# Optimization experiments

Measured on AMD Instinct MI355X. Metric: run time of the kernel, lower is better.

## Reference

```python
import jax, jax.numpy as jnp
import numpy as np

B, K, N, DIM, C_IN = 4, 2048, 4096, 3, 61
IN = DIM + C_IN        # 64, deepset input size
H1, H2 = 128, 128      # neighbor_xf hidden sizes
OUT = 64               # c_out // heads
HEADS = 4
EPS = 1e-5             # BatchNorm eps


def _lin(key, i, o):
    return jax.random.normal(key, (i, o), jnp.float32) * (1.0 / np.sqrt(i))


def setup_inputs() -> dict:
    key = jax.random.key(0)
    ks = jax.random.split(key, 12)
    return {
        "keys": jax.random.normal(ks[0], (B, K, DIM), jnp.float32),
        "points": jax.random.normal(ks[1], (B, N, DIM), jnp.float32),
        "feats": jax.random.normal(ks[2], (B, N, C_IN), jnp.float32),
        "nx_w1": _lin(ks[3], IN, H1), "nx_b1": jnp.zeros((H1,), jnp.float32),
        "nx_w2": _lin(ks[4], H1, H2), "nx_b2": jnp.zeros((H2,), jnp.float32),
        "nx_w3": _lin(ks[5], H2, OUT), "nx_b3": jnp.zeros((OUT,), jnp.float32),
        "sx_w1": _lin(ks[6], IN, IN), "sx_b1": jnp.zeros((IN,), jnp.float32),
        "sx_w2": _lin(ks[7], IN, IN), "sx_b2": jnp.zeros((IN,), jnp.float32),
        "sx_w3": _lin(ks[8], IN, IN), "sx_b3": jnp.zeros((IN,), jnp.float32),
        "att_w": _lin(ks[9], 2 * IN, HEADS * IN),
        "att_b": jnp.zeros((HEADS * IN,), jnp.float32),
        "att_q": jax.random.normal(ks[10], (HEADS, IN), jnp.float32) * 0.1,
        "bn_gamma": jnp.ones((IN,), jnp.float32),
        "bn_beta": jnp.zeros((IN,), jnp.float32),
        "neighbors": 32,
    }


def _mlp3(x, w1, b1, w2, b2, w3, b3):
    # per-element deepset MLP: Linear-ReLU-Linear-ReLU-Linear
    h = jax.nn.relu(x @ w1 + b1)
    h = jax.nn.relu(h @ w2 + b2)
    return h @ w3 + b3


def _forward(keys, points, feats, nx_w1, nx_b1, nx_w2, nx_b2, nx_w3, nx_b3,
             sx_w1, sx_b1, sx_w2, sx_b2, sx_w3, sx_b3,
             att_w, att_b, att_q, bn_gamma, bn_beta, neighbors):
    b = keys.shape[0]
    # Euclidean dist_fn: dist_vec [B,K,N,dim], dist [B,K,N], all points valid
    rel = points[:, None, :, :] - keys[:, :, None, :]
    dist = jnp.sqrt(jnp.sum(rel * rel, axis=-1))
    _, idx = jax.lax.top_k(-dist, neighbors)                   # [B,K,k] nearest
    nrel = jnp.take_along_axis(rel, idx[..., None], axis=2)    # [B,K,k,dim]
    bidx = jnp.arange(b)[:, None, None]
    nfeat = feats[bidx, idx]                                   # [B,K,k,c_in]
    comb = jnp.concatenate([nrel, nfeat], axis=-1)             # [B,K,k,in]
    lat = _mlp3(comb, nx_w1, nx_b1, nx_w2, nx_b2, nx_w3, nx_b3)  # [B,K,k,out]
    # BatchNorm1d (training-mode batch stats) over flattened [B*K*k, in]
    flat = comb.reshape(-1, comb.shape[-1])
    mean = jnp.mean(flat, axis=0)
    var = jnp.var(flat, axis=0)
    norm = (comb - mean) * jax.lax.rsqrt(var + EPS) * bn_gamma + bn_beta
    # SelfAttention: deepset sum-pooled context + per-neighbor softmax weights
    set_feat = jnp.sum(_mlp3(norm, sx_w1, sx_b1, sx_w2, sx_b2, sx_w3, sx_b3), axis=2)
    comb_feat = jnp.concatenate(
        [norm, jnp.broadcast_to(set_feat[:, :, None, :], norm.shape)], axis=-1)
    heads = (comb_feat @ att_w + att_b).reshape(comb_feat.shape[:3] + (HEADS, -1))
    e = jnp.sum(heads * att_q, axis=-1)                        # [B,K,k,H]
    w = jax.nn.softmax(e, axis=-2)                             # softmax over neighbor axis
    out = jnp.einsum('bkno,bknh->bkoh', lat, w)                # weighted reduce over k
    return out.reshape(out.shape[:2] + (-1,))                  # [B,K,out*H]


def reference(keys, points, feats, nx_w1, nx_b1, nx_w2, nx_b2, nx_w3, nx_b3,
              sx_w1, sx_b1, sx_w2, sx_b2, sx_w3, sx_b3,
              att_w, att_b, att_q, bn_gamma, bn_beta, neighbors):
    return _forward(keys, points, feats, nx_w1, nx_b1, nx_w2, nx_b2, nx_w3, nx_b3,
                    sx_w1, sx_b1, sx_w2, sx_b2, sx_w3, sx_b3,
                    att_w, att_b, att_q, bn_gamma, bn_beta, neighbors)
```

## Files before the change

kernel.cpp:

```cpp
#include <hip/hip_runtime.h>
#include <math.h>

#define BATCH 4
#define KQ    2048
#define NPTS  4096
#define CIN   61
#define KNN   32
#define ROWS  (BATCH*KQ*KNN)

#define OFF_IDX  0
#define OFF_ACC  524288
#define OFF_ATTA 557056
#define OFF_W1F  558080
#define OFF_W2F  574464
#define OFF_W3F  607232

typedef __attribute__((ext_vector_type(8)))  short bfrag;
typedef __attribute__((ext_vector_type(16))) float cfrag;

__device__ __forceinline__ unsigned short bf16_rne(float x) {
  unsigned u = __float_as_uint(x);
  unsigned r = u + 0x7fffu + ((u >> 16) & 1u);
  return (unsigned short)(r >> 16);
}
__device__ __forceinline__ float4 ld4u(const float* p) {
  float4 r; __builtin_memcpy(&r, p, 16); return r;
}

#define NCAND 320

template<int NS>
__device__ __forceinline__ void select_emit(
    const unsigned* __restrict__ VAL, const int* __restrict__ IDXL,
    int mcount, unsigned hib, int lane, int wid,
    const float* __restrict__ Pb, float kx, float ky, float kz,
    unsigned short* __restrict__ dst, int* __restrict__ SEL,
    float* __restrict__ accs) {
  const unsigned long long lmask = (1ull << lane) - 1ull;
  unsigned e[NS];
#pragma unroll
  for (int s = 0; s < NS; ++s) {
    int ei = s*64 + lane;
    e[s] = (ei < mcount) ? VAL[ei] : 0xffffffffu;
  }
  unsigned lo2 = e[0];
#pragma unroll
  for (int s = 1; s < NS; ++s) lo2 = min(lo2, e[s]);
#pragma unroll
  for (int off = 1; off < 64; off <<= 1)
    lo2 = min(lo2, (unsigned)__shfl_xor((int)lo2, off));
  unsigned hi2 = hib;
  while (lo2 < hi2) {
    unsigned mid = lo2 + ((hi2 - lo2) >> 1);
    int c = 0;
#pragma unroll
    for (int s = 0; s < NS; ++s) c += (int)__popcll(__ballot(e[s] <= mid));
    if (c == KNN) { hi2 = mid; break; }
    if (c > KNN) hi2 = mid; else lo2 = mid + 1;
  }
  const unsigned T = hi2;
  float r0=0.f,r1=0.f,r2=0.f,r3=0.f,r4=0.f,r5=0.f;
  int base2 = 0;
#pragma unroll
  for (int s = 0; s < NS; ++s) {
    bool p = (e[s] <= T);
    unsigned long long m = __ballot(p);
    if (p) {
      int pos = base2 + (int)__popcll(m & lmask);
      if (pos < KNN) {
        int n = IDXL[s*64 + lane];
        SEL[pos] = n;
        if (wid == 0) {
          dst[pos] = (unsigned short)n;
          float dx = Pb[n*3+0]-kx, dy = Pb[n*3+1]-ky, dz = Pb[n*3+2]-kz;
          r0 += dx; r1 += dy; r2 += dz;
          r3 += dx*dx; r4 += dy*dy; r5 += dz*dz;
        }
      }
    }
    base2 += (int)__popcll(m);
  }
  if (wid == 0) {
#pragma unroll
    for (int off = 32; off > 0; off >>= 1) {
      r0 += __shfl_down(r0, off); r1 += __shfl_down(r1, off);
      r2 += __shfl_down(r2, off); r3 += __shfl_down(r3, off);
      r4 += __shfl_down(r4, off); r5 += __shfl_down(r5, off);
    }
    if (lane == 0) {
      atomicAdd(&accs[0], r0); atomicAdd(&accs[1], r1); atomicAdd(&accs[2], r2);
      atomicAdd(&accs[64], r3); atomicAdd(&accs[65], r4); atomicAdd(&accs[66], r5);
    }
  }
}

__global__ __launch_bounds__(256, 8) void topk_kernel(
    const float* __restrict__ keys, const float* __restrict__ points,
    const float* __restrict__ feats,
    const float* __restrict__ w1, const float* __restrict__ w2,
    const float* __restrict__ w3,
    const float* __restrict__ att_w, const float* __restrict__ att_q,
    unsigned short* __restrict__ idx_out, float* __restrict__ acc,
    short* __restrict__ w1f, short* __restrict__ w2f, short* __restrict__ w3f,
    float* __restrict__ attA) {
  if (blockIdx.x >= 8192) {
    const int bb = blockIdx.x - 8192;
    if (bb == 128) {
      const int t = threadIdx.x, c = t >> 2, h = t & 3;
      float s = 0.f;
      for (int d = 0; d < 64; ++d) s += att_w[c*256 + h*64 + d] * att_q[h*64 + d];
      attA[c*4 + h] = s;
      return;
    }
    int t = bb * 256 + threadIdx.x;
    if (t < 8192) {
      int j = t & 7, lane = (t >> 3) & 63, tk = t >> 9;
      int kc = tk & 3, tile = tk >> 2;
      int nh = tile*32 + (lane & 31), k = kc*16 + (lane >> 5)*8 + j;
      w1f[t] = (short)bf16_rne(w1[k*128 + nh]);
    } else if (t < 24576) {
      int t2 = t - 8192;
      int j = t2 & 7, lane = (t2 >> 3) & 63, tk = t2 >> 9;
      int kc = tk & 7, tile = tk >> 3;
      int nh = tile*32 + (lane & 31), k = kc*16 + (lane >> 5)*8 + j;
      w2f[t2] = (short)bf16_rne(w2[k*128 + nh]);
    } else {
      int t3 = t - 24576;
      int j = t3 & 7, lane = (t3 >> 3) & 63, tk = t3 >> 9;
      int kc = tk & 7, tile = tk >> 3;
      int nh = tile*32 + (lane & 31), k = kc*16 + (lane >> 5)*8 + j;
      w3f[t3] = (short)bf16_rne(w3[k*64 + nh]);
    }
    return;
  }

  __shared__ unsigned VAL[NCAND];
  __shared__ int IDXL[NCAND];
  __shared__ int SEL[32];
  __shared__ unsigned HIW[4];
  __shared__ int WTOT[4];
  __shared__ float FRED[64*33];
  __shared__ float FQ[64*33];
  const int tid = threadIdx.x;
  const int lane = tid & 63, wid = tid >> 6;
  const int g = blockIdx.x;
  const int b = g >> 11;
  const float kx = keys[(size_t)g*3+0];
  const float ky = keys[(size_t)g*3+1];
  const float kz = keys[(size_t)g*3+2];
  const float* __restrict__ Pb = points + (size_t)b * NPTS * 3;

  unsigned u[16];
  unsigned lmin = 0xffffffffu;
#pragma unroll
  for (int c4 = 0; c4 < 4; ++c4) {
    const float* pp = Pb + (size_t)(tid*16 + c4*4) * 3;
    float4 A = ld4u(pp), B = ld4u(pp + 4), C = ld4u(pp + 8);
    float dx, dy, dz;
    dx = A.x-kx; dy = A.y-ky; dz = A.z-kz;
    u[c4*4+0] = __float_as_uint(dx*dx + dy*dy + dz*dz);
    dx = A.w-kx; dy = B.x-ky; dz = B.y-kz;
    u[c4*4+1] = __float_as_uint(dx*dx + dy*dy + dz*dz);
    dx = B.z-kx; dy = B.w-ky; dz = C.x-kz;
    u[c4*4+2] = __float_as_uint(dx*dx + dy*dy + dz*dz);
    dx = C.y-kx; dy = C.z-ky; dz = C.w-kz;
    u[c4*4+3] = __float_as_uint(dx*dx + dy*dy + dz*dz);
#pragma unroll
    for (int j = 0; j < 4; ++j) lmin = min(lmin, u[c4*4+j]);
  }
  unsigned wlo = lmin, whi = lmin;
#pragma unroll
  for (int off = 1; off < 64; off <<= 1) {
    unsigned a = (unsigned)__shfl_xor((int)wlo, off);
    unsigned bmx = (unsigned)__shfl_xor((int)whi, off);
    wlo = min(wlo, a); whi = max(whi, bmx);
  }
  unsigned lo = wlo, hi = whi;
  while (lo < hi) {
    unsigned mid = lo + ((hi - lo) >> 1);
    int c = (int)__popcll(__ballot(lmin <= mid));
    if (c == KNN) { hi = mid; break; }
    if (c > KNN) hi = mid; else lo = mid + 1;
  }
  if (lane == 0) HIW[wid] = hi;
  __syncthreads();
  const unsigned hib = min(min(HIW[0],HIW[1]), min(HIW[2],HIW[3]));

  int cnt = 0;
#pragma unroll
  for (int j = 0; j < 16; ++j) cnt += (u[j] <= hib) ? 1 : 0;
  int inc = cnt;
#pragma unroll
  for (int off = 1; off < 64; off <<= 1) {
    int t = __shfl_up(inc, off);
    if (lane >= off) inc += t;
  }
  if (lane == 63) WTOT[wid] = inc;
  __syncthreads();
  int base = inc - cnt;
  for (int w = 0; w < wid; ++w) base += WTOT[w];
  {
    int p = base;
#pragma unroll
    for (int j = 0; j < 16; ++j) {
      if (u[j] <= hib) {
        if (p < NCAND) { VAL[p] = u[j]; IDXL[p] = tid*16 + j; }
        ++p;
      }
    }
  }
  __syncthreads();
  const int mcount = min(WTOT[0]+WTOT[1]+WTOT[2]+WTOT[3], NCAND);

  {
    unsigned short* dst = idx_out + (size_t)g * KNN;
    float* accs = &acc[(g & 63)*128];
    if (mcount <= 64)
      select_emit<1>(VAL, IDXL, mcount, hib, lane, wid, Pb, kx, ky, kz, dst, SEL, accs);
    else if (mcount <= 128)
      select_emit<2>(VAL, IDXL, mcount, hib, lane, wid, Pb, kx, ky, kz, dst, SEL, accs);
    else
      select_emit<5>(VAL, IDXL, mcount, hib, lane, wid, Pb, kx, ky, kz, dst, SEL, accs);
  }

  {
    const int row = tid >> 3, chunk = tid & 7;
    const int n = SEL[row];
    const float* frow = feats + ((size_t)b*NPTS + n)*CIN;
    float fs[8] = {0,0,0,0,0,0,0,0}, fq[8] = {0,0,0,0,0,0,0,0};
    if (chunk < 7) {
      float4 a = ld4u(frow + chunk*8);
      float4 c4 = ld4u(frow + chunk*8 + 4);
      fs[0]=a.x;  fq[0]=a.x*a.x;   fs[1]=a.y;  fq[1]=a.y*a.y;
      fs[2]=a.z;  fq[2]=a.z*a.z;   fs[3]=a.w;  fq[3]=a.w*a.w;
      fs[4]=c4.x; fq[4]=c4.x*c4.x; fs[5]=c4.y; fq[5]=c4.y*c4.y;
      fs[6]=c4.z; fq[6]=c4.z*c4.z; fs[7]=c4.w; fq[7]=c4.w*c4.w;
    } else {
      float v0=frow[56], v1=frow[57], v2=frow[58], v3=frow[59], v4=frow[60];
      fs[0]=v0; fq[0]=v0*v0; fs[1]=v1; fq[1]=v1*v1;
      fs[2]=v2; fq[2]=v2*v2; fs[3]=v3; fq[3]=v3*v3;
      fs[4]=v4; fq[4]=v4*v4;
    }
#pragma unroll
    for (int i = 0; i < 8; ++i) {
      FRED[(chunk*8 + i)*33 + row] = fs[i];
      FQ  [(chunk*8 + i)*33 + row] = fq[i];
    }
  }
  __syncthreads();
  if (tid < 64) {
    float s = 0.f, q2 = 0.f;
#pragma unroll
    for (int r = 0; r < 32; ++r) {
      s  += FRED[tid*33 + r];
      q2 += FQ[tid*33 + r];
    }
    if (tid < CIN) {
      float* a = &acc[(g & 63)*128];
      atomicAdd(&a[3 + tid], s);
      atomicAdd(&a[64 + 3 + tid], q2);
    }
  }
}

#define L_W1F 0
#define L_W2F 16384
#define L_W3F 49152
#define L_B1  65536
#define L_B2  66048
#define L_B3  66560
#define L_AE  66816
#define L_ACT 67840
#define L_EPX 137472
#define L_TOT 145664

template<int KC, bool F32OUT>
__device__ __forceinline__ void gemm_part(const short* WF,
    const float* BIAS, short* ACTq, float* LATq,
    const bfrag* B, int tile0, int ntiles, int m, int q, int lane) {
#pragma unroll
  for (int t = 0; t < ntiles; ++t) {
    const int tile = tile0 + t;
    cfrag acc;
#pragma unroll
    for (int i = 0; i < 16; ++i) acc[i] = 0.f;
#pragma unroll
    for (int kc = 0; kc < KC; ++kc) {
      bfrag a = *(const bfrag*)(WF + ((tile*KC + kc)*64 + lane)*8);
      acc = __builtin_amdgcn_mfma_f32_32x32x16_bf16(a, B[kc], acc, 0, 0, 0);
    }
#pragma unroll
    for (int p = 0; p < 4; ++p) {
      const int nh = tile*32 + p*8 + q*4;
      float4 bv = *(const float4*)(BIAS + nh);
      if (F32OUT) {
        float4 o;
        o.x = acc[4*p+0] + bv.x; o.y = acc[4*p+1] + bv.y;
        o.z = acc[4*p+2] + bv.z; o.w = acc[4*p+3] + bv.w;
        *(float4*)(LATq + m*68 + nh) = o;
      } else {
        short4 s;
        s.x = (short)bf16_rne(fmaxf(acc[4*p+0] + bv.x, 0.f));
        s.y = (short)bf16_rne(fmaxf(acc[4*p+1] + bv.y, 0.f));
        s.z = (short)bf16_rne(fmaxf(acc[4*p+2] + bv.z, 0.f));
        s.w = (short)bf16_rne(fmaxf(acc[4*p+3] + bv.w, 0.f));
        *(short4*)(ACTq + m*136 + nh) = s;
      }
    }
  }
}

__global__ __launch_bounds__(1024, 4) void main_kernel(
    const float* __restrict__ keys, const float* __restrict__ points,
    const float* __restrict__ feats, const unsigned short* __restrict__ idxg,
    const short* __restrict__ w1f, const short* __restrict__ w2f,
    const short* __restrict__ w3f,
    const float* __restrict__ b1, const float* __restrict__ b2,
    const float* __restrict__ b3,
    const float* __restrict__ attAg, const float* __restrict__ accg,
    const float* __restrict__ gammav, float* __restrict__ out) {
  __shared__ __align__(16) char smem[L_TOT];
  const int tid = threadIdx.x;
  const int bid = blockIdx.x;
  const int wid = tid >> 6, lane = tid & 63;
  const int pairq = wid >> 1, wv = wid & 1;
  const int m = lane & 31, q = lane >> 5;

  short* SW1 = (short*)(smem + L_W1F);
  short* SW2 = (short*)(smem + L_W2F);
  short* SW3 = (short*)(smem + L_W3F);
  float* SB1 = (float*)(smem + L_B1);
  float* SB2 = (float*)(smem + L_B2);
  float* SB3 = (float*)(smem + L_B3);
  float* SAe = (float*)(smem + L_AE);
  short* ACTq = (short*)(smem + L_ACT + pairq * 8704);
  float* LATq = (float*)(smem + L_ACT + pairq * 8704);
  float* EPX  = (float*)(smem + L_EPX) + pairq * 256;

  {
    ((uint4*)SW1)[tid] = ((const uint4*)w1f)[tid];
    ((uint4*)SW2)[tid] = ((const uint4*)w2f)[tid];
    ((uint4*)SW2)[tid + 1024] = ((const uint4*)w2f)[tid + 1024];
    ((uint4*)SW3)[tid] = ((const uint4*)w3f)[tid];
    if (tid < 128) SB1[tid] = b1[tid];
    else if (tid < 256) SB2[tid-128] = b2[tid-128];
    else if (tid < 320) SB3[tid-256] = b3[tid-256];
    float* TMP = (float*)(smem + L_ACT);
    if (tid < 512) {
      int c = tid & 63, p = tid >> 6;
      float s = 0.f, s2 = 0.f;
      for (int k = p; k < 64; k += 8) {
        s += accg[k*128 + c]; s2 += accg[k*128 + 64 + c];
      }
      TMP[p*128 + c] = s; TMP[p*128 + 64 + c] = s2;
    }
    __syncthreads();
    float* SCt = (float*)(smem + L_EPX);
    if (tid < 64) {
      float s = 0.f, s2 = 0.f;
#pragma unroll
      for (int p = 0; p < 8; ++p) { s += TMP[p*128 + tid]; s2 += TMP[p*128 + 64 + tid]; }
      const float invR = 1.f / (float)ROWS;
      float mean = s * invR;
      float var = s2 * invR - mean * mean;
      SCt[tid] = gammav[tid] * rsqrtf(var + 1e-5f);
    }
    __syncthreads();
    if (tid < 256) SAe[tid] = attAg[tid] * SCt[tid >> 2];
    __syncthreads();
  }

  auto load_gather = [&](int grp2, float* v) {
    const int g2 = grp2 * 8 + pairq;
    const int bq2 = g2 >> 11;
    const int c0 = wv*32 + q*16;
    const int n = (int)idxg[(size_t)g2*KNN + m];
    const float* frow = feats + ((size_t)bq2*NPTS + n)*CIN;
    if (wv == 0 && q == 0) {
      const float* Pb = points + (size_t)bq2 * NPTS * 3;
      v[0] = Pb[n*3+0] - keys[(size_t)g2*3+0];
      v[1] = Pb[n*3+1] - keys[(size_t)g2*3+1];
      v[2] = Pb[n*3+2] - keys[(size_t)g2*3+2];
#pragma unroll
      for (int kk = 0; kk < 3; ++kk) {
        float4 t = ld4u(frow + kk*4);
        v[3+kk*4+0] = t.x; v[3+kk*4+1] = t.y; v[3+kk*4+2] = t.z; v[3+kk*4+3] = t.w;
      }
      v[15] = frow[12];
    } else {
      const int base = c0 - 3;
#pragma unroll
      for (int kk = 0; kk < 4; ++kk) {
        float4 t = ld4u(frow + base + kk*4);
        v[kk*4+0] = t.x; v[kk*4+1] = t.y; v[kk*4+2] = t.z; v[kk*4+3] = t.w;
      }
    }
  };

  float vcur[16];
  load_gather(bid, vcur);

  for (int grp = bid; grp < BATCH*KQ/8; grp += 256) {
    const int g = grp * 8 + pairq;
    const int c0 = wv*32 + q*16;

    {
      float ep0 = 0.f, ep1 = 0.f, ep2 = 0.f, ep3 = 0.f;
#pragma unroll
      for (int cc = 0; cc < 16; ++cc) {
        float4 ae = *(const float4*)(SAe + (c0 + cc)*4);
        ep0 = fmaf(vcur[cc], ae.x, ep0);
        ep1 = fmaf(vcur[cc], ae.y, ep1);
        ep2 = fmaf(vcur[cc], ae.z, ep2);
        ep3 = fmaf(vcur[cc], ae.w, ep3);
      }
      ep0 += __shfl_xor(ep0, 32); ep1 += __shfl_xor(ep1, 32);
      ep2 += __shfl_xor(ep2, 32); ep3 += __shfl_xor(ep3, 32);
#pragma unroll
      for (int k = 0; k < 2; ++k) {
        bfrag pk;
#pragma unroll
        for (int t = 0; t < 8; ++t) pk[t] = (short)bf16_rne(vcur[k*8 + t]);
        *(bfrag*)(ACTq + m*136 + c0 + k*8) = pk;
      }
      if (q == 0) {
        float4 e4; e4.x = ep0; e4.y = ep1; e4.z = ep2; e4.w = ep3;
        *(float4*)(EPX + m*8 + wv*4) = e4;
      }
    }
    __syncthreads();

    float vnext[16];
    const int gnext = grp + 256;
    if (gnext < BATCH*KQ/8) load_gather(gnext, vnext);

    if (wv == 0) {
      const int h0 = q*2;
      float ea = EPX[m*8 + h0]     + EPX[m*8 + 4 + h0];
      float eb = EPX[m*8 + h0 + 1] + EPX[m*8 + 5 + h0];
      float ma = ea, mb = eb;
#pragma unroll
      for (int off = 1; off < 32; off <<= 1) {
        ma = fmaxf(ma, __shfl_xor(ma, off));
        mb = fmaxf(mb, __shfl_xor(mb, off));
      }
      float xa = __expf(ea - ma), xb = __expf(eb - mb);
      float sa = xa, sb = xb;
#pragma unroll
      for (int off = 1; off < 32; off <<= 1) {
        sa += __shfl_xor(sa, off);
        sb += __shfl_xor(sb, off);
      }
      EPX[m*8 + h0]     = xa / sa;
      EPX[m*8 + h0 + 1] = xb / sb;
    }

    {
      bfrag B4[4];
#pragma unroll
      for (int kc = 0; kc < 4; ++kc)
        B4[kc] = *(const bfrag*)(ACTq + m*136 + kc*16 + q*8);
      __syncthreads();
      gemm_part<4, false>(SW1, SB1, ACTq, LATq, B4, wv*2, 2, m, q, lane);
    }
    __syncthreads();
    {
      bfrag B8[8];
#pragma unroll
      for (int kc = 0; kc < 8; ++kc)
        B8[kc] = *(const bfrag*)(ACTq + m*136 + kc*16 + q*8);
      __syncthreads();
      gemm_part<8, false>(SW2, SB2, ACTq, LATq, B8, wv*2, 2, m, q, lane);
    }
    __syncthreads();
    {
      bfrag C8[8];
#pragma unroll
      for (int kc = 0; kc < 8; ++kc)
        C8[kc] = *(const bfrag*)(ACTq + m*136 + kc*16 + q*8);
      __syncthreads();
      gemm_part<8, true>(SW3, SB3, ACTq, LATq, C8, wv, 1, m, q, lane);
    }
    __syncthreads();

    {
      const int oi = wv*64 + lane;
      const int o = oi >> 1, hp = oi & 1;
      float a0 = 0.f, a1 = 0.f;
#pragma unroll
      for (int n2 = 0; n2 < KNN; ++n2) {
        float l = LATq[n2*68 + o];
        float2 wv2 = *(const float2*)(EPX + n2*8 + hp*2);
        a0 = fmaf(l, wv2.x, a0);
        a1 = fmaf(l, wv2.y, a1);
      }
      float2 r; r.x = a0; r.y = a1;
      *(float2*)(out + (size_t)g*256 + o*4 + hp*2) = r;
    }
    __syncthreads();

#pragma unroll
    for (int i = 0; i < 16; ++i) vcur[i] = vnext[i];
  }
}

extern "C" void kernel_launch(void* const* d_in, const int* in_sizes, int n_in,
                              void* d_out, int out_size, void* d_ws, size_t ws_size,
                              hipStream_t stream) {
  const float* keys   = (const float*)d_in[0];
  const float* points = (const float*)d_in[1];
  const float* feats  = (const float*)d_in[2];
  const float* nx_w1  = (const float*)d_in[3];
  const float* nx_b1  = (const float*)d_in[4];
  const float* nx_w2  = (const float*)d_in[5];
  const float* nx_b2  = (const float*)d_in[6];
  const float* nx_w3  = (const float*)d_in[7];
  const float* nx_b3  = (const float*)d_in[8];
  const float* att_w  = (const float*)d_in[15];
  const float* att_q  = (const float*)d_in[17];
  const float* gamma  = (const float*)d_in[18];
  float* out = (float*)d_out;

  char* ws = (char*)d_ws;
  unsigned short* idxp = (unsigned short*)(ws + OFF_IDX);
  float* acc  = (float*)(ws + OFF_ACC);
  float* attA = (float*)(ws + OFF_ATTA);
  short* w1f  = (short*)(ws + OFF_W1F);
  short* w2f  = (short*)(ws + OFF_W2F);
  short* w3f  = (short*)(ws + OFF_W3F);

  hipMemsetAsync(acc, 0, 32768, stream);
  topk_kernel<<<8192 + 129, 256, 0, stream>>>(keys, points, feats,
      nx_w1, nx_w2, nx_w3, att_w, att_q, idxp, acc, w1f, w2f, w3f, attA);
  main_kernel<<<256, 1024, 0, stream>>>(keys, points, feats, idxp,
      w1f, w2f, w3f, nx_b1, nx_b2, nx_b3, attA, acc, gamma, out);
}
```

Before: 197.7 us.

## Process two query keys per top-k block to reuse point loads

```diff
diff --git a/kernel.cpp b/kernel.cpp
--- a/kernel.cpp
+++ b/kernel.cpp
@@ -32,7 +32,7 @@
 template<int NS>
 __device__ __forceinline__ void select_emit(
     const unsigned* __restrict__ VAL, const int* __restrict__ IDXL,
-    int mcount, unsigned hib, int lane, int wid,
+    int mcount, unsigned hib, unsigned lob, int lane,
     const float* __restrict__ Pb, float kx, float ky, float kz,
     unsigned short* __restrict__ dst, int* __restrict__ SEL,
     float* __restrict__ accs) {
@@ -43,13 +43,7 @@
     int ei = s*64 + lane;
     e[s] = (ei < mcount) ? VAL[ei] : 0xffffffffu;
   }
-  unsigned lo2 = e[0];
-#pragma unroll
-  for (int s = 1; s < NS; ++s) lo2 = min(lo2, e[s]);
-#pragma unroll
-  for (int off = 1; off < 64; off <<= 1)
-    lo2 = min(lo2, (unsigned)__shfl_xor((int)lo2, off));
-  unsigned hi2 = hib;
+  unsigned lo2 = lob, hi2 = hib;
   while (lo2 < hi2) {
     unsigned mid = lo2 + ((hi2 - lo2) >> 1);
     int c = 0;
@@ -70,31 +64,39 @@
       if (pos < KNN) {
         int n = IDXL[s*64 + lane];
         SEL[pos] = n;
-        if (wid == 0) {
-          dst[pos] = (unsigned short)n;
-          float dx = Pb[n*3+0]-kx, dy = Pb[n*3+1]-ky, dz = Pb[n*3+2]-kz;
-          r0 += dx; r1 += dy; r2 += dz;
-          r3 += dx*dx; r4 += dy*dy; r5 += dz*dz;
-        }
+        dst[pos] = (unsigned short)n;
+        float dx = Pb[n*3+0]-kx, dy = Pb[n*3+1]-ky, dz = Pb[n*3+2]-kz;
+        r0 += dx; r1 += dy; r2 += dz;
+        r3 += dx*dx; r4 += dy*dy; r5 += dz*dz;
       }
     }
     base2 += (int)__popcll(m);
   }
-  if (wid == 0) {
-#pragma unroll
-    for (int off = 32; off > 0; off >>= 1) {
-      r0 += __shfl_down(r0, off); r1 += __shfl_down(r1, off);
-      r2 += __shfl_down(r2, off); r3 += __shfl_down(r3, off);
-      r4 += __shfl_down(r4, off); r5 += __shfl_down(r5, off);
-    }
-    if (lane == 0) {
-      atomicAdd(&accs[0], r0); atomicAdd(&accs[1], r1); atomicAdd(&accs[2], r2);
-      atomicAdd(&accs[64], r3); atomicAdd(&accs[65], r4); atomicAdd(&accs[66], r5);
-    }
-  }
-}
-
-__global__ __launch_bounds__(256, 8) void topk_kernel(
+#pragma unroll
+  for (int off = 32; off > 0; off >>= 1) {
+    r0 += __shfl_down(r0, off); r1 += __shfl_down(r1, off);
+    r2 += __shfl_down(r2, off); r3 += __shfl_down(r3, off);
+    r4 += __shfl_down(r4, off); r5 += __shfl_down(r5, off);
+  }
+  if (lane == 0) {
+    atomicAdd(&accs[0], r0); atomicAdd(&accs[1], r1); atomicAdd(&accs[2], r2);
+    atomicAdd(&accs[64], r3); atomicAdd(&accs[65], r4); atomicAdd(&accs[66], r5);
+  }
+}
+
+__device__ __forceinline__ void dispatch_select(
+    const unsigned* VAL, const int* IDXL, int mcount, unsigned hib, unsigned lob,
+    int lane, const float* Pb, float kx, float ky, float kz,
+    unsigned short* dst, int* SEL, float* accs) {
+  if (mcount <= 64)
+    select_emit<1>(VAL, IDXL, mcount, hib, lob, lane, Pb, kx, ky, kz, dst, SEL, accs);
+  else if (mcount <= 128)
+    select_emit<2>(VAL, IDXL, mcount, hib, lob, lane, Pb, kx, ky, kz, dst, SEL, accs);
+  else
+    select_emit<5>(VAL, IDXL, mcount, hib, lob, lane, Pb, kx, ky, kz, dst, SEL, accs);
+}
+
+__global__ __launch_bounds__(256, 6) void topk_kernel(
     const float* __restrict__ keys, const float* __restrict__ points,
     const float* __restrict__ feats,
     const float* __restrict__ w1, const float* __restrict__ w2,
@@ -103,8 +105,8 @@
     unsigned short* __restrict__ idx_out, float* __restrict__ acc,
     short* __restrict__ w1f, short* __restrict__ w2f, short* __restrict__ w3f,
     float* __restrict__ attA) {
-  if (blockIdx.x >= 8192) {
-    const int bb = blockIdx.x - 8192;
+  if (blockIdx.x >= 4096) {
+    const int bb = blockIdx.x - 4096;
     if (bb == 128) {
       const int t = threadIdx.x, c = t >> 2, h = t & 3;
       float s = 0.f;
@@ -134,112 +136,149 @@
     return;
   }
 
-  __shared__ unsigned VAL[NCAND];
-  __shared__ int IDXL[NCAND];
-  __shared__ int SEL[32];
-  __shared__ unsigned HIW[4];
-  __shared__ int WTOT[4];
+  __shared__ unsigned VAL[2][NCAND];
+  __shared__ int IDXL[2][NCAND];
+  __shared__ int SEL[2][KNN];
+  __shared__ unsigned HIW[2][4], LOW[2][4];
+  __shared__ int WTOT[2][4];
   __shared__ float FRED[64*33];
   __shared__ float FQ[64*33];
   const int tid = threadIdx.x;
   const int lane = tid & 63, wid = tid >> 6;
-  const int g = blockIdx.x;
-  const int b = g >> 11;
-  const float kx = keys[(size_t)g*3+0];
-  const float ky = keys[(size_t)g*3+1];
-  const float kz = keys[(size_t)g*3+2];
+  const int g0 = blockIdx.x * 2, g1 = g0 + 1;
+  const int b = g0 >> 11;
+  const float kxA = keys[(size_t)g0*3+0], kyA = keys[(size_t)g0*3+1], kzA = keys[(size_t)g0*3+2];
+  const float kxB = keys[(size_t)g1*3+0], kyB = keys[(size_t)g1*3+1], kzB = keys[(size_t)g1*3+2];
   const float* __restrict__ Pb = points + (size_t)b * NPTS * 3;
 
-  unsigned u[16];
-  unsigned lmin = 0xffffffffu;
+  unsigned uA[16], uB[16];
+  unsigned lminA = 0xffffffffu, lminB = 0xffffffffu;
 #pragma unroll
   for (int c4 = 0; c4 < 4; ++c4) {
     const float* pp = Pb + (size_t)(tid*16 + c4*4) * 3;
-    float4 A = ld4u(pp), B = ld4u(pp + 4), C = ld4u(pp + 8);
-    float dx, dy, dz;
-    dx = A.x-kx; dy = A.y-ky; dz = A.z-kz;
-    u[c4*4+0] = __float_as_uint(dx*dx + dy*dy + dz*dz);
-    dx = A.w-kx; dy = B.x-ky; dz = B.y-kz;
-    u[c4*4+1] = __float_as_uint(dx*dx + dy*dy + dz*dz);
-    dx = B.z-kx; dy = B.w-ky; dz = C.x-kz;
-    u[c4*4+2] = __float_as_uint(dx*dx + dy*dy + dz*dz);
-    dx = C.y-kx; dy = C.z-ky; dz = C.w-kz;
-    u[c4*4+3] = __float_as_uint(dx*dx + dy*dy + dz*dz);
-#pragma unroll
-    for (int j = 0; j < 4; ++j) lmin = min(lmin, u[c4*4+j]);
-  }
-  unsigned wlo = lmin, whi = lmin;
+    float4 A = ld4u(pp), B4 = ld4u(pp + 4), C4 = ld4u(pp + 8);
+    float x, y, z, dx, dy, dz;
+#define DPT(slot, PX, PY, PZ)                                        \
+    x = PX; y = PY; z = PZ;                                          \
+    dx = x-kxA; dy = y-kyA; dz = z-kzA;                              \
+    uA[slot] = __float_as_uint(dx*dx + dy*dy + dz*dz);               \
+    lminA = min(lminA, uA[slot]);                                    \
+    dx = x-kxB; dy = y-kyB; dz = z-kzB;                              \
+    uB[slot] = __float_as_uint(dx*dx + dy*dy + dz*dz);               \
+    lminB = min(lminB, uB[slot]);
+    DPT(c4*4+0, A.x,  A.y,  A.z)
+    DPT(c4*4+1, A.w,  B4.x, B4.y)
+    DPT(c4*4+2, B4.z, B4.w, C4.x)
+    DPT(c4*4+3, C4.y, C4.z, C4.w)
+#undef DPT
+  }
+  unsigned wloA = lminA, whiA = lminA, wloB = lminB, whiB = lminB;
 #pragma unroll
   for (int off = 1; off < 64; off <<= 1) {
-    unsigned a = (unsigned)__shfl_xor((int)wlo, off);
-    unsigned bmx = (unsigned)__shfl_xor((int)whi, off);
-    wlo = min(wlo, a); whi = max(whi, bmx);
-  }
-  unsigned lo = wlo, hi = whi;
-  while (lo < hi) {
-    unsigned mid = lo + ((hi - lo) >> 1);
-    int c = (int)__popcll(__ballot(lmin <= mid));
-    if (c == KNN) { hi = mid; break; }
-    if (c > KNN) hi = mid; else lo = mid + 1;
-  }
-  if (lane == 0) HIW[wid] = hi;
+    unsigned a0 = (unsigned)__shfl_xor((int)wloA, off);
+    unsigned a1 = (unsigned)__shfl_xor((int)whiA, off);
+    unsigned b0 = (unsigned)__shfl_xor((int)wloB, off);
+    unsigned b1 = (unsigned)__shfl_xor((int)whiB, off);
+    wloA = min(wloA, a0); whiA = max(whiA, a1);
+    wloB = min(wloB, b0); whiB = max(whiB, b1);
+  }
+  unsigned hiA, hiB;
+  {
+    unsigned lo = wloA, hi = whiA;
+    while (lo < hi) {
+      unsigned mid = lo + ((hi - lo) >> 1);
+      int c = (int)__popcll(__ballot(lminA <= mid));
+      if (c == KNN) { hi = mid; break; }
+      if (c > KNN) hi = mid; else lo = mid + 1;
+    }
+    hiA = hi;
+    lo = wloB; hi = whiB;
+    while (lo < hi) {
+      unsigned mid = lo + ((hi - lo) >> 1);
+      int c = (int)__popcll(__ballot(lminB <= mid));
+      if (c == KNN) { hi = mid; break; }
+      if (c > KNN) hi = mid; else lo = mid + 1;
+    }
+    hiB = hi;
+  }
+  if (lane == 0) {
+    HIW[0][wid] = hiA; HIW[1][wid] = hiB;
+    LOW[0][wid] = wloA; LOW[1][wid] = wloB;
+  }
   __syncthreads();
-  const unsigned hib = min(min(HIW[0],HIW[1]), min(HIW[2],HIW[3]));
-
-  int cnt = 0;
-#pragma unroll
-  for (int j = 0; j < 16; ++j) cnt += (u[j] <= hib) ? 1 : 0;
-  int inc = cnt;
+  const unsigned hibA = min(min(HIW[0][0],HIW[0][1]), min(HIW[0][2],HIW[0][3]));
+  const unsigned hibB = min(min(HIW[1][0],HIW[1][1]), min(HIW[1][2],HIW[1][3]));
+  const unsigned lobA = min(min(LOW[0][0],LOW[0][1]), min(LOW[0][2],LOW[0][3]));
+  const unsigned lobB = min(min(LOW[1][0],LOW[1][1]), min(LOW[1][2],LOW[1][3]));
+
+  int cntA = 0, cntB = 0;
+#pragma unroll
+  for (int j = 0; j < 16; ++j) {
+    cntA += (uA[j] <= hibA) ? 1 : 0;
+    cntB += (uB[j] <= hibB) ? 1 : 0;
+  }
+  int incA = cntA, incB = cntB;
 #pragma unroll
   for (int off = 1; off < 64; off <<= 1) {
-    int t = __shfl_up(inc, off);
-    if (lane >= off) inc += t;
-  }
-  if (lane == 63) WTOT[wid] = inc;
+    int tA = __shfl_up(incA, off);
+    int tB = __shfl_up(incB, off);
+    if (lane >= off) { incA += tA; incB += tB; }
+  }
+  if (lane == 63) { WTOT[0][wid] = incA; WTOT[1][wid] = incB; }
   __syncthreads();
-  int base = inc - cnt;
-  for (int w = 0; w < wid; ++w) base += WTOT[w];
+  int baseA = incA - cntA, baseB = incB - cntB;
+  for (int w = 0; w < wid; ++w) { baseA += WTOT[0][w]; baseB += WTOT[1][w]; }
   {
-    int p = base;
+    int pA = baseA, pB = baseB;
 #pragma unroll
     for (int j = 0; j < 16; ++j) {
-      if (u[j] <= hib) {
-        if (p < NCAND) { VAL[p] = u[j]; IDXL[p] = tid*16 + j; }
-        ++p;
+      if (uA[j] <= hibA) {
+        if (pA < NCAND) { VAL[0][pA] = uA[j]; IDXL[0][pA] = tid*16 + j; }
+        ++pA;
+      }
+      if (uB[j] <= hibB) {
+        if (pB < NCAND) { VAL[1][pB] = uB[j]; IDXL[1][pB] = tid*16 + j; }
+        ++pB;
       }
     }
   }
   __syncthreads();
-  const int mcount = min(WTOT[0]+WTOT[1]+WTOT[2]+WTOT[3], NCAND);
-
-  {
-    unsigned short* dst = idx_out + (size_t)g * KNN;
-    float* accs = &acc[(g & 63)*128];
-    if (mcount <= 64)
-      select_emit<1>(VAL, IDXL, mcount, hib, lane, wid, Pb, kx, ky, kz, dst, SEL, accs);
-    else if (mcount <= 128)
-      select_emit<2>(VAL, IDXL, mcount, hib, lane, wid, Pb, kx, ky, kz, dst, SEL, accs);
-    else
-      select_emit<5>(VAL, IDXL, mcount, hib, lane, wid, Pb, kx, ky, kz, dst, SEL, accs);
-  }
+  const int mcountA = min(WTOT[0][0]+WTOT[0][1]+WTOT[0][2]+WTOT[0][3], NCAND);
+  const int mcountB = min(WTOT[1][0]+WTOT[1][1]+WTOT[1][2]+WTOT[1][3], NCAND);
+
+  float* accs = &acc[(blockIdx.x & 63)*128];
+  if (wid == 0) {
+    dispatch_select(VAL[0], IDXL[0], mcountA, hibA, lobA, lane, Pb,
+                    kxA, kyA, kzA, idx_out + (size_t)g0*KNN, SEL[0], accs);
+  } else if (wid == 2) {
+    dispatch_select(VAL[1], IDXL[1], mcountB, hibB, lobB, lane, Pb,
+                    kxB, kyB, kzB, idx_out + (size_t)g1*KNN, SEL[1], accs);
+  }
+  __syncthreads();
 
   {
     const int row = tid >> 3, chunk = tid & 7;
-    const int n = SEL[row];
-    const float* frow = feats + ((size_t)b*NPTS + n)*CIN;
+    const int nA = SEL[0][row], nB = SEL[1][row];
+    const float* frA = feats + ((size_t)b*NPTS + nA)*CIN;
+    const float* frB = feats + ((size_t)b*NPTS + nB)*CIN;
     float fs[8] = {0,0,0,0,0,0,0,0}, fq[8] = {0,0,0,0,0,0,0,0};
     if (chunk < 7) {
-      float4 a = ld4u(frow + chunk*8);
-      float4 c4 = ld4u(frow + chunk*8 + 4);
-      fs[0]=a.x;  fq[0]=a.x*a.x;   fs[1]=a.y;  fq[1]=a.y*a.y;
-      fs[2]=a.z;  fq[2]=a.z*a.z;   fs[3]=a.w;  fq[3]=a.w*a.w;
-      fs[4]=c4.x; fq[4]=c4.x*c4.x; fs[5]=c4.y; fq[5]=c4.y*c4.y;
-      fs[6]=c4.z; fq[6]=c4.z*c4.z; fs[7]=c4.w; fq[7]=c4.w*c4.w;
+      float4 a0 = ld4u(frA + chunk*8), a1 = ld4u(frA + chunk*8 + 4);
+      float4 b0 = ld4u(frB + chunk*8), b1 = ld4u(frB + chunk*8 + 4);
+      fs[0]=a0.x+b0.x; fq[0]=a0.x*a0.x+b0.x*b0.x;
+      fs[1]=a0.y+b0.y; fq[1]=a0.y*a0.y+b0.y*b0.y;
+      fs[2]=a0.z+b0.z; fq[2]=a0.z*a0.z+b0.z*b0.z;
+      fs[3]=a0.w+b0.w; fq[3]=a0.w*a0.w+b0.w*b0.w;
+      fs[4]=a1.x+b1.x; fq[4]=a1.x*a1.x+b1.x*b1.x;
+      fs[5]=a1.y+b1.y; fq[5]=a1.y*a1.y+b1.y*b1.y;
+      fs[6]=a1.z+b1.z; fq[6]=a1.z*a1.z+b1.z*b1.z;
+      fs[7]=a1.w+b1.w; fq[7]=a1.w*a1.w+b1.w*b1.w;
     } else {
-      float v0=frow[56], v1=frow[57], v2=frow[58], v3=frow[59], v4=frow[60];
-      fs[0]=v0; fq[0]=v0*v0; fs[1]=v1; fq[1]=v1*v1;
-      fs[2]=v2; fq[2]=v2*v2; fs[3]=v3; fq[3]=v3*v3;
-      fs[4]=v4; fq[4]=v4*v4;
+#pragma unroll
+      for (int i = 0; i < 5; ++i) {
+        float va = frA[56+i], vb = frB[56+i];
+        fs[i] = va + vb; fq[i] = va*va + vb*vb;
+      }
     }
 #pragma unroll
     for (int i = 0; i < 8; ++i) {
@@ -256,9 +295,8 @@
       q2 += FQ[tid*33 + r];
     }
     if (tid < CIN) {
-      float* a = &acc[(g & 63)*128];
-      atomicAdd(&a[3 + tid], s);
-      atomicAdd(&a[64 + 3 + tid], q2);
+      atomicAdd(&accs[3 + tid], s);
+      atomicAdd(&accs[64 + 3 + tid], q2);
     }
   }
 }
@@ -530,7 +568,7 @@
   short* w3f  = (short*)(ws + OFF_W3F);
 
   hipMemsetAsync(acc, 0, 32768, stream);
-  topk_kernel<<<8192 + 129, 256, 0, stream>>>(keys, points, feats,
+  topk_kernel<<<4096 + 129, 256, 0, stream>>>(keys, points, feats,
       nx_w1, nx_w2, nx_w3, att_w, att_q, idxp, acc, w1f, w2f, w3f, attA);
   main_kernel<<<256, 1024, 0, stream>>>(keys, points, feats, idxp,
       w1f, w2f, w3f, nx_b1, nx_b2, nx_b3, attA, acc, gamma, out);
```

New measurement: 183.3 us. 7.3% less time.
